# Performance work log

Hardware: AMD Instinct MI355X
Metric: run time of the kernel (lower is better)

## Reference

```python
import jax, jax.numpy as jnp
import numpy as np

EPS = 1e-6

def _rmsnorm(x, w):
    # matches RMSNorm: compute in fp32, cast back, then scale by weight
    dt = x.dtype
    xf = x.astype(jnp.float32)
    var = jnp.mean(xf * xf, axis=-1, keepdims=True)
    xf = xf * jax.lax.rsqrt(var + EPS)
    return xf.astype(dt) * w


def setup_inputs() -> dict:
    key = jax.random.key(0)
    ks = jax.random.split(key, 4)
    B, N, C = 4, 2048, 1024
    H = 16
    D = C // H
    x = jax.random.normal(ks[0], (B, N, C), dtype=jnp.float32)
    W_qkv = jax.random.normal(ks[1], (C, 3 * C), dtype=jnp.float32) * (1.0 / np.sqrt(C))
    b_qkv = jnp.zeros((3 * C,), dtype=jnp.float32)
    W_proj = jax.random.normal(ks[2], (C, C), dtype=jnp.float32) * (1.0 / np.sqrt(C))
    b_proj = jnp.zeros((C,), dtype=jnp.float32)
    qn_w = jnp.ones((D,), dtype=jnp.float32)
    kn_w = jnp.ones((D,), dtype=jnp.float32)
    return {"x": x, "W_qkv": W_qkv, "b_qkv": b_qkv, "W_proj": W_proj,
            "b_proj": b_proj, "qn_w": qn_w, "kn_w": kn_w}


def reference(x, W_qkv, b_qkv, W_proj, b_proj, qn_w, kn_w):
    B, N, C = x.shape
    H = 16
    D = C // H
    qkv = jnp.einsum('bnc,cd->bnd', x, W_qkv) + b_qkv          # [B,N,3C]
    qkv = qkv.reshape(B, N, 3, H, D)
    q = qkv[:, :, 0].transpose(0, 2, 1, 3)                     # [B,H,N,D]
    k = qkv[:, :, 1].transpose(0, 2, 1, 3)
    v = qkv[:, :, 2].transpose(0, 2, 1, 3)
    q = _rmsnorm(q, qn_w)
    k = _rmsnorm(k, kn_w)
    scale = D ** -0.5
    attn = jnp.einsum('bhqd,bhkd->bhqk', q, k) * scale         # [B,H,N,N]
    attn = jax.nn.softmax(attn, axis=-1)
    out = jnp.einsum('bhqk,bhkd->bhqd', attn, v)               # [B,H,N,D]
    out = out.transpose(0, 2, 1, 3).reshape(B, N, C)
    out = jnp.einsum('bnc,cd->bnd', out, W_proj) + b_proj
    return out
```

## Files before the change

### kernel.cpp

```cpp
#include <hip/hip_runtime.h>
#include <stdint.h>

#define B_ 4
#define N_ 2048
#define C_ 1024
#define H_ 16
#define D_ 64
#define M_ (B_*N_)
#define N3_ (3*C_)

typedef __attribute__((ext_vector_type(8))) __bf16 bf16x8;
typedef bf16x8 bf16x8_ma __attribute__((may_alias));
typedef __attribute__((ext_vector_type(4))) float floatx4;
typedef unsigned short u16;
typedef unsigned int u32;

typedef __attribute__((address_space(1))) const void void_g;
typedef __attribute__((address_space(3))) void void_l;

__device__ __forceinline__ void glds16(const void* g, void* l) {
  __builtin_amdgcn_global_load_lds((void_g*)g, (void_l*)l, 16, 0, 0);
}

__device__ __forceinline__ u16 f2bf(float f) {
  union { float f; u32 u; } x; x.f = f;
  u32 r = x.u + 0x7fffu + ((x.u >> 16) & 1u);
  return (u16)(r >> 16);
}

__device__ __forceinline__ float fexp2(float x) {
#if __has_builtin(__builtin_amdgcn_exp2f)
  return __builtin_amdgcn_exp2f(x);
#else
  return exp2f(x);
#endif
}

__global__ __launch_bounds__(256)
void convert_x(const float4* __restrict__ in, uint2* __restrict__ out, int n4) {
  int idx = blockIdx.x * 256 + threadIdx.x;
  if (idx >= n4) return;
  float4 v = in[idx];
  union { u16 a[4]; uint2 u; } p;
  p.a[0] = f2bf(v.x); p.a[1] = f2bf(v.y); p.a[2] = f2bf(v.z); p.a[3] = f2bf(v.w);
  out[idx] = p.u;
}

__global__ __launch_bounds__(256)
void transpose_cvt(const float* __restrict__ in, u16* __restrict__ out,
                   int R, int Ccols) {
  __shared__ u16 tile[64][65];
  int c0 = blockIdx.x * 64, r0 = blockIdx.y * 64;
  int tid = threadIdx.x;
#pragma unroll
  for (int it = 0; it < 16; ++it) {
    int idx = it * 256 + tid;
    int r = idx >> 6, c = idx & 63;
    tile[c][r] = f2bf(in[(size_t)(r0 + r) * Ccols + c0 + c]);
  }
  __syncthreads();
#pragma unroll
  for (int it = 0; it < 16; ++it) {
    int idx = it * 256 + tid;
    int oc = idx >> 6, orr = idx & 63;
    out[(size_t)(c0 + oc) * R + r0 + orr] = tile[oc][orr];
  }
}

__global__ __launch_bounds__(256)
void transpose_v(const u16* __restrict__ qkv, u16* __restrict__ vt) {
  __shared__ u16 tile[64][65];
  int bh = blockIdx.y, b = bh >> 4, h = bh & 15;
  int n0 = blockIdx.x * 64;
  int tid = threadIdx.x;
#pragma unroll
  for (int it = 0; it < 16; ++it) {
    int idx = it * 256 + tid;
    int n = idx >> 6, d = idx & 63;
    tile[d][n] = qkv[(size_t)(b * N_ + n0 + n) * N3_ + 2 * C_ + h * D_ + d];
  }
  __syncthreads();
#pragma unroll
  for (int it = 0; it < 16; ++it) {
    int idx = it * 256 + tid;
    int d = idx >> 6, n = idx & 63;
    int np = (n & 0x23) | ((n & 0x0C) << 1) | ((n & 0x10) >> 2);
    vt[(size_t)(bh * D_ + d) * N_ + n0 + np] = tile[d][n];
  }
}

__global__ __launch_bounds__(512, 2)
void gemm_qkv_256(const u16* __restrict__ A, const u16* __restrict__ Bt,
                  const float* __restrict__ bias, u16* __restrict__ Cout,
                  const float* __restrict__ qn, const float* __restrict__ kn) {
  __shared__ __align__(16) u16 sA[4][16 * 512];
  __shared__ __align__(16) u16 sB[4][16 * 512];
  const int K = C_;
  int tid = threadIdx.x;
  int wave = tid >> 6, lane = tid & 63;
  int lrow = lane & 15, lq = lane >> 4;
  int n0 = blockIdx.x * 256;
  int m0 = blockIdx.y * 256;
  int wm = wave >> 2, wn = wave & 3;

  floatx4 acc[8][4];
#pragma unroll
  for (int i = 0; i < 8; ++i)
#pragma unroll
    for (int j = 0; j < 4; ++j) acc[i][j] = (floatx4){0.f, 0.f, 0.f, 0.f};

  const u16* pa0 = A  + (size_t)(m0 + (2 * wave + 0) * 16 + lrow) * K + lq * 8;
  const u16* pa1 = A  + (size_t)(m0 + (2 * wave + 1) * 16 + lrow) * K + lq * 8;
  const u16* pb0 = Bt + (size_t)(n0 + (2 * wave + 0) * 16 + lrow) * K + lq * 8;
  const u16* pb1 = Bt + (size_t)(n0 + (2 * wave + 1) * 16 + lrow) * K + lq * 8;
  int oa0 = (2 * wave + 0) * 512, oa1 = (2 * wave + 1) * 512;

#define STAGE_HK(hk_)                                   \
  do {                                                  \
    int s_ = (hk_) & 3;                                 \
    int ko_ = (hk_) * 32;                               \
    glds16(pa0 + ko_, &sA[s_][oa0]);                    \
    glds16(pa1 + ko_, &sA[s_][oa1]);                    \
    glds16(pb0 + ko_, &sB[s_][oa0]);                    \
    glds16(pb1 + ko_, &sB[s_][oa1]);                    \
  } while (0)

  STAGE_HK(0); STAGE_HK(1); STAGE_HK(2);

  for (int hk = 0; hk < 32; ++hk) {
    if (hk < 30)       asm volatile("s_waitcnt vmcnt(8)" ::: "memory");
    else if (hk == 30) asm volatile("s_waitcnt vmcnt(4)" ::: "memory");
    else               asm volatile("s_waitcnt vmcnt(0)" ::: "memory");
    __builtin_amdgcn_s_barrier();
    asm volatile("" ::: "memory");

    if (hk + 3 < 32) STAGE_HK(hk + 3);

    int s = hk & 3;
    bf16x8 af[8], bfr[4];
#pragma unroll
    for (int i = 0; i < 8; ++i)
      af[i] = *(const bf16x8_ma*)(&sA[s][(wm * 8 + i) * 512 + lane * 8]);
#pragma unroll
    for (int j = 0; j < 4; ++j)
      bfr[j] = *(const bf16x8_ma*)(&sB[s][(wn * 4 + j) * 512 + lane * 8]);

    __builtin_amdgcn_s_setprio(1);
#pragma unroll
    for (int i = 0; i < 8; ++i)
#pragma unroll
      for (int j = 0; j < 4; ++j)
        acc[i][j] = __builtin_amdgcn_mfma_f32_16x16x32_bf16(af[i], bfr[j], acc[i][j], 0, 0, 0);
    __builtin_amdgcn_s_setprio(0);
  }
#undef STAGE_HK

  int colbase = n0 + wn * 64;
  float bv[4];
#pragma unroll
  for (int j = 0; j < 4; ++j) bv[j] = bias[colbase + j * 16 + lrow];
#pragma unroll
  for (int i = 0; i < 8; ++i)
#pragma unroll
    for (int j = 0; j < 4; ++j)
#pragma unroll
      for (int r = 0; r < 4; ++r) acc[i][j][r] += bv[j];

  int sect = colbase >> 10;
  if (sect < 2) {
    const float* wptr = (sect == 0) ? qn : kn;
    float wv[4];
#pragma unroll
    for (int j = 0; j < 4; ++j) wv[j] = wptr[j * 16 + lrow];
#pragma unroll
    for (int i = 0; i < 8; ++i)
#pragma unroll
      for (int r = 0; r < 4; ++r) {
        float ss = 0.f;
#pragma unroll
        for (int j = 0; j < 4; ++j) { float v = acc[i][j][r]; ss += v * v; }
        ss += __shfl_xor(ss, 1);
        ss += __shfl_xor(ss, 2);
        ss += __shfl_xor(ss, 4);
        ss += __shfl_xor(ss, 8);
        float rstd = rsqrtf(ss * (1.0f / 64.0f) + 1e-6f);
#pragma unroll
        for (int j = 0; j < 4; ++j) acc[i][j][r] *= rstd * wv[j];
      }
  }

#pragma unroll
  for (int i = 0; i < 8; ++i)
#pragma unroll
    for (int j = 0; j < 4; ++j)
#pragma unroll
      for (int r = 0; r < 4; ++r) {
        int row = m0 + wm * 128 + i * 16 + lq * 4 + r;
        int col = colbase + j * 16 + lrow;
        Cout[(size_t)row * N3_ + col] = f2bf(acc[i][j][r]);
      }
}

__global__ __launch_bounds__(256)
void gemm_bt(const u16* __restrict__ A, const u16* __restrict__ Bt,
             const float* __restrict__ bias, void* __restrict__ Cout,
             int Ncols, int lda, int do_rms, int out_fp32,
             const float* __restrict__ qn, const float* __restrict__ kn) {
  __shared__ __align__(16) u16 sA[3][8 * 512];
  __shared__ __align__(16) u16 sB[3][8 * 512];
  const int K = C_;
  int tid = threadIdx.x;
  int wave = tid >> 6, lane = tid & 63;
  int lrow = lane & 15, lq = lane >> 4;
  int n0 = blockIdx.x * 128;
  int m0 = blockIdx.y * 128;
  int wm = wave >> 1, wn = wave & 1;

  floatx4 acc[4][4];
#pragma unroll
  for (int i = 0; i < 4; ++i)
#pragma unroll
    for (int j = 0; j < 4; ++j) acc[i][j] = (floatx4){0.f, 0.f, 0.f, 0.f};

  const u16* ga0 = A  + (size_t)(m0 + (2 * wave + 0) * 16 + lrow) * lda + lq * 8;
  const u16* ga1 = A  + (size_t)(m0 + (2 * wave + 1) * 16 + lrow) * lda + lq * 8;
  const u16* gb0 = Bt + (size_t)(n0 + (2 * wave + 0) * 16 + lrow) * K + lq * 8;
  const u16* gb1 = Bt + (size_t)(n0 + (2 * wave + 1) * 16 + lrow) * K + lq * 8;
  int o0 = (2 * wave + 0) * 512;
  int o1 = (2 * wave + 1) * 512;

  u16* aA = &sA[0][0]; u16* aB = &sA[1][0]; u16* aC = &sA[2][0];
  u16* bA = &sB[0][0]; u16* bB = &sB[1][0]; u16* bC = &sB[2][0];

  glds16(ga0, aA + o0); glds16(ga1, aA + o1);
  glds16(gb0, bA + o0); glds16(gb1, bA + o1);
  glds16(ga0 + 32, aB + o0); glds16(ga1 + 32, aB + o1);
  glds16(gb0 + 32, bB + o0); glds16(gb1 + 32, bB + o1);

  for (int kt = 0; kt < K; kt += 32) {
    if (kt + 32 < K) {
      asm volatile("s_waitcnt vmcnt(4)" ::: "memory");
    } else {
      asm volatile("s_waitcnt vmcnt(0)" ::: "memory");
    }
    __builtin_amdgcn_s_barrier();
    asm volatile("" ::: "memory");

    if (kt + 64 < K) {
      glds16(ga0 + kt + 64, aC + o0);
      glds16(ga1 + kt + 64, aC + o1);
      glds16(gb0 + kt + 64, bC + o0);
      glds16(gb1 + kt + 64, bC + o1);
    }

    bf16x8 af[4], bfr[4];
#pragma unroll
    for (int i = 0; i < 4; ++i)
      af[i] = *(const bf16x8_ma*)(aA + (wm * 4 + i) * 512 + lane * 8);
#pragma unroll
    for (int j = 0; j < 4; ++j)
      bfr[j] = *(const bf16x8_ma*)(bA + (wn * 4 + j) * 512 + lane * 8);
#pragma unroll
    for (int i = 0; i < 4; ++i)
#pragma unroll
      for (int j = 0; j < 4; ++j)
        acc[i][j] = __builtin_amdgcn_mfma_f32_16x16x32_bf16(af[i], bfr[j], acc[i][j], 0, 0, 0);

    u16* t;
    t = aA; aA = aB; aB = aC; aC = t;
    t = bA; bA = bB; bB = bC; bC = t;
  }

  int colbase = n0 + wn * 64;
  float bv[4];
#pragma unroll
  for (int j = 0; j < 4; ++j) bv[j] = bias[colbase + j * 16 + lrow];
#pragma unroll
  for (int i = 0; i < 4; ++i)
#pragma unroll
    for (int j = 0; j < 4; ++j)
#pragma unroll
      for (int r = 0; r < 4; ++r) acc[i][j][r] += bv[j];

  int sect = colbase >> 10;
  if (do_rms && sect < 2) {
    const float* wptr = (sect == 0) ? qn : kn;
    float wv[4];
#pragma unroll
    for (int j = 0; j < 4; ++j) wv[j] = wptr[j * 16 + lrow];
#pragma unroll
    for (int i = 0; i < 4; ++i)
#pragma unroll
      for (int r = 0; r < 4; ++r) {
        float ss = 0.f;
#pragma unroll
        for (int j = 0; j < 4; ++j) { float v = acc[i][j][r]; ss += v * v; }
        ss += __shfl_xor(ss, 1);
        ss += __shfl_xor(ss, 2);
        ss += __shfl_xor(ss, 4);
        ss += __shfl_xor(ss, 8);
        float rstd = rsqrtf(ss * (1.0f / 64.0f) + 1e-6f);
#pragma unroll
        for (int j = 0; j < 4; ++j) acc[i][j][r] *= rstd * wv[j];
      }
  }

#pragma unroll
  for (int i = 0; i < 4; ++i)
#pragma unroll
    for (int j = 0; j < 4; ++j)
#pragma unroll
      for (int r = 0; r < 4; ++r) {
        int row = m0 + wm * 64 + i * 16 + lq * 4 + r;
        int col = colbase + j * 16 + lrow;
        if (out_fp32)
          ((float*)Cout)[(size_t)row * Ncols + col] = acc[i][j][r];
        else
          ((u16*)Cout)[(size_t)row * Ncols + col] = f2bf(acc[i][j][r]);
      }
}

__global__ __launch_bounds__(256)
void flash_attn(u16* __restrict__ qkv, const u16* __restrict__ vt) {
  __shared__ __align__(16) u16 sK[2][8 * 512];
  __shared__ __align__(16) u16 sV[2][8 * 512];
  int tid = threadIdx.x;
  int wave = tid >> 6, lane = tid & 63;
  int lrow = lane & 15, lq = lane >> 4;
  int bh = blockIdx.y, b = bh >> 4, h = bh & 15;
  int q0 = blockIdx.x * 128;
  const float cc = 0.125f * 1.44269504088896340736f;

  bf16x8 qf[2][2];
#pragma unroll
  for (int i = 0; i < 2; ++i)
#pragma unroll
    for (int kq = 0; kq < 2; ++kq) {
      union { bf16x8 v; __bf16 e[8]; } t;
      t.v = *(const bf16x8_ma*)(qkv +
          (size_t)(b * N_ + q0 + wave * 32 + i * 16 + lrow) * N3_ +
          h * D_ + kq * 32 + lq * 8);
#pragma unroll
      for (int e = 0; e < 8; ++e) t.e[e] = (__bf16)((float)t.e[e] * cc);
      qf[i][kq] = t.v;
    }

  union { bf16x8 v; u16 e[8]; } one_;
#pragma unroll
  for (int e = 0; e < 8; ++e) one_.e[e] = 0x3F80;
  bf16x8 onef = one_.v;

  floatx4 aco[2][4];
  floatx4 acl[2];
#pragma unroll
  for (int i = 0; i < 2; ++i) {
#pragma unroll
    for (int nd = 0; nd < 4; ++nd) aco[i][nd] = (floatx4){0.f, 0.f, 0.f, 0.f};
    acl[i] = (floatx4){0.f, 0.f, 0.f, 0.f};
  }

  const u16* gk[2];
  const u16* gv[2];
#pragma unroll
  for (int t = 0; t < 2; ++t) {
    int blk = wave * 2 + t;
    int j = blk >> 1, kq = blk & 1;
    gk[t] = qkv + (size_t)(b * N_ + j * 16 + lrow) * N3_ +
            C_ + h * D_ + kq * 32 + lq * 8;
    gv[t] = vt + (size_t)(bh * D_ + j * 16 + lrow) * N_ + kq * 32 + lq * 8;
  }

  u16* k_cur = &sK[0][0]; u16* k_nxt = &sK[1][0];
  u16* v_cur = &sV[0][0]; u16* v_nxt = &sV[1][0];

#pragma unroll
  for (int t = 0; t < 2; ++t) {
    int blk = wave * 2 + t;
    glds16(gk[t], k_cur + blk * 512);
    glds16(gv[t], v_cur + blk * 512);
  }
  __syncthreads();

  for (int kt = 0; kt < 32; ++kt) {
    if (kt < 31) {
      size_t key0n = (size_t)(kt + 1) * 64;
#pragma unroll
      for (int t = 0; t < 2; ++t) {
        int blk = wave * 2 + t;
        glds16(gk[t] + key0n * N3_, k_nxt + blk * 512);
        glds16(gv[t] + key0n, v_nxt + blk * 512);
      }
    }

    floatx4 accs[2][4];
    __builtin_amdgcn_s_setprio(1);
#pragma unroll
    for (int j = 0; j < 4; ++j) {
      bf16x8 kf0 = *(const bf16x8_ma*)(k_cur + (j * 2 + 0) * 512 + lane * 8);
      bf16x8 kf1 = *(const bf16x8_ma*)(k_cur + (j * 2 + 1) * 512 + lane * 8);
#pragma unroll
      for (int i = 0; i < 2; ++i) {
        floatx4 s = (floatx4){0.f, 0.f, 0.f, 0.f};
        s = __builtin_amdgcn_mfma_f32_16x16x32_bf16(kf0, qf[i][0], s, 0, 0, 0);
        s = __builtin_amdgcn_mfma_f32_16x16x32_bf16(kf1, qf[i][1], s, 0, 0, 0);
        accs[i][j] = s;
      }
    }
    __builtin_amdgcn_s_setprio(0);

    bf16x8 pf[2][2];
#pragma unroll
    for (int i = 0; i < 2; ++i) {
      union { bf16x8 v; __bf16 e[8]; } pk0, pk1;
#pragma unroll
      for (int j = 0; j < 4; ++j)
#pragma unroll
        for (int r = 0; r < 4; ++r) {
          float p = fexp2(accs[i][j][r]);
          if (j < 2) pk0.e[(j & 1) * 4 + r] = (__bf16)p;
          else       pk1.e[(j & 1) * 4 + r] = (__bf16)p;
        }
      pf[i][0] = pk0.v;
      pf[i][1] = pk1.v;
    }

    __builtin_amdgcn_s_setprio(1);
#pragma unroll
    for (int kq = 0; kq < 2; ++kq) {
#pragma unroll
      for (int nd = 0; nd < 4; ++nd) {
        bf16x8 vf = *(const bf16x8_ma*)(v_cur + (nd * 2 + kq) * 512 + lane * 8);
        aco[0][nd] = __builtin_amdgcn_mfma_f32_16x16x32_bf16(vf, pf[0][kq], aco[0][nd], 0, 0, 0);
        aco[1][nd] = __builtin_amdgcn_mfma_f32_16x16x32_bf16(vf, pf[1][kq], aco[1][nd], 0, 0, 0);
      }
      acl[0] = __builtin_amdgcn_mfma_f32_16x16x32_bf16(onef, pf[0][kq], acl[0], 0, 0, 0);
      acl[1] = __builtin_amdgcn_mfma_f32_16x16x32_bf16(onef, pf[1][kq], acl[1], 0, 0, 0);
    }
    __builtin_amdgcn_s_setprio(0);

    __syncthreads();
    u16* t0 = k_cur; k_cur = k_nxt; k_nxt = t0;
    u16* t1 = v_cur; v_cur = v_nxt; v_nxt = t1;
  }

#pragma unroll
  for (int i = 0; i < 2; ++i) {
    float inv = 1.0f / acl[i][0];
    int row = q0 + wave * 32 + i * 16 + lrow;
#pragma unroll
    for (int nd = 0; nd < 4; ++nd) {
      union { u16 a[4]; uint2 u; } st;
#pragma unroll
      for (int r = 0; r < 4; ++r) st.a[r] = f2bf(aco[i][nd][r] * inv);
      *(uint2*)(qkv + (size_t)(b * N_ + row) * N3_ + h * D_ + nd * 16 + lq * 4) = st.u;
    }
  }
}

extern "C" void kernel_launch(void* const* d_in, const int* in_sizes, int n_in,
                              void* d_out, int out_size, void* d_ws, size_t ws_size,
                              hipStream_t stream) {
  (void)in_sizes; (void)n_in; (void)out_size; (void)ws_size;
  const float* x     = (const float*)d_in[0];
  const float* Wqkv  = (const float*)d_in[1];
  const float* bqkv  = (const float*)d_in[2];
  const float* Wproj = (const float*)d_in[3];
  const float* bproj = (const float*)d_in[4];
  const float* qn    = (const float*)d_in[5];
  const float* kn    = (const float*)d_in[6];
  float* out = (float*)d_out;

  char* ws = (char*)d_ws;
  u16* xb      = (u16*)ws;  ws += (size_t)M_ * C_ * 2;
  u16* Wt_qkv  = (u16*)ws;  ws += (size_t)N3_ * C_ * 2;
  u16* Wt_proj = (u16*)ws;  ws += (size_t)C_ * C_ * 2;
  u16* qkv     = (u16*)ws;  ws += (size_t)M_ * N3_ * 2;
  u16* vt      = (u16*)ws;  ws += (size_t)B_ * H_ * D_ * N_ * 2;

  convert_x<<<dim3(M_ * C_ / 4 / 256), 256, 0, stream>>>(
      (const float4*)x, (uint2*)xb, M_ * C_ / 4);
  transpose_cvt<<<dim3(N3_ / 64, C_ / 64), 256, 0, stream>>>(Wqkv, Wt_qkv, C_, N3_);
  transpose_cvt<<<dim3(C_ / 64, C_ / 64), 256, 0, stream>>>(Wproj, Wt_proj, C_, C_);
  gemm_qkv_256<<<dim3(N3_ / 256, M_ / 256), 512, 0, stream>>>(
      xb, Wt_qkv, bqkv, qkv, qn, kn);
  transpose_v<<<dim3(N_ / 64, B_ * H_), 256, 0, stream>>>(qkv, vt);
  flash_attn<<<dim3(N_ / 128, B_ * H_), 256, 0, stream>>>(qkv, vt);
  gemm_bt<<<dim3(C_ / 128, M_ / 128), 256, 0, stream>>>(
      qkv, Wt_proj, bproj, out, C_, N3_, 0, 1, qn, kn);
}
```

Measured before the change: 340.1 us.

## Shrink QKV GEMM tile to 128x256 and add XCD-aware block swizzling

Replaces the 256x256 QKV GEMM, which used a 4-stage pipeline and setprio, with a 128x256 tile on a 3-stage LDS pipeline. This halves the accumulators per wave and doubles the number of workgroups. It also remaps block indices in the projection GEMM and flash attention so that consecutive logical tiles land on the same XCD, aiming for better L2 reuse. The smaller tile lowers arithmetic intensity per block and drops the priority hints, in exchange for more parallelism and lower register pressure.

```diff
diff --git a/kernel.cpp b/kernel.cpp
--- a/kernel.cpp
+++ b/kernel.cpp
@@ -34,6 +34,11 @@
 #else
   return exp2f(x);
 #endif
+}
+
+__device__ __forceinline__ int xcd_swz(int hw, int nwg) {
+  int per = nwg >> 3;
+  return (hw & 7) * per + (hw >> 3);
 }
 
 __global__ __launch_bounds__(256)
@@ -89,78 +94,81 @@
   }
 }
 
-__global__ __launch_bounds__(512, 2)
-void gemm_qkv_256(const u16* __restrict__ A, const u16* __restrict__ Bt,
-                  const float* __restrict__ bias, u16* __restrict__ Cout,
-                  const float* __restrict__ qn, const float* __restrict__ kn) {
-  __shared__ __align__(16) u16 sA[4][16 * 512];
-  __shared__ __align__(16) u16 sB[4][16 * 512];
+__global__ __launch_bounds__(512)
+void gemm_qkv(const u16* __restrict__ A, const u16* __restrict__ Bt,
+              const float* __restrict__ bias, u16* __restrict__ Cout,
+              const float* __restrict__ qn, const float* __restrict__ kn) {
+  __shared__ __align__(16) u16 sA[3][8 * 512];
+  __shared__ __align__(16) u16 sB[3][16 * 512];
   const int K = C_;
   int tid = threadIdx.x;
   int wave = tid >> 6, lane = tid & 63;
   int lrow = lane & 15, lq = lane >> 4;
   int n0 = blockIdx.x * 256;
-  int m0 = blockIdx.y * 256;
+  int m0 = blockIdx.y * 128;
   int wm = wave >> 2, wn = wave & 3;
 
-  floatx4 acc[8][4];
-#pragma unroll
-  for (int i = 0; i < 8; ++i)
+  floatx4 acc[4][4];
+#pragma unroll
+  for (int i = 0; i < 4; ++i)
 #pragma unroll
     for (int j = 0; j < 4; ++j) acc[i][j] = (floatx4){0.f, 0.f, 0.f, 0.f};
 
-  const u16* pa0 = A  + (size_t)(m0 + (2 * wave + 0) * 16 + lrow) * K + lq * 8;
-  const u16* pa1 = A  + (size_t)(m0 + (2 * wave + 1) * 16 + lrow) * K + lq * 8;
-  const u16* pb0 = Bt + (size_t)(n0 + (2 * wave + 0) * 16 + lrow) * K + lq * 8;
-  const u16* pb1 = Bt + (size_t)(n0 + (2 * wave + 1) * 16 + lrow) * K + lq * 8;
-  int oa0 = (2 * wave + 0) * 512, oa1 = (2 * wave + 1) * 512;
-
-#define STAGE_HK(hk_)                                   \
-  do {                                                  \
-    int s_ = (hk_) & 3;                                 \
-    int ko_ = (hk_) * 32;                               \
-    glds16(pa0 + ko_, &sA[s_][oa0]);                    \
-    glds16(pa1 + ko_, &sA[s_][oa1]);                    \
-    glds16(pb0 + ko_, &sB[s_][oa0]);                    \
-    glds16(pb1 + ko_, &sB[s_][oa1]);                    \
+  const u16* ga  = A  + (size_t)(m0 + wave * 16 + lrow) * K + lq * 8;
+  const u16* gb0 = Bt + (size_t)(n0 + (2 * wave + 0) * 16 + lrow) * K + lq * 8;
+  const u16* gb1 = Bt + (size_t)(n0 + (2 * wave + 1) * 16 + lrow) * K + lq * 8;
+  int oa  = wave * 512;
+  int ob0 = (2 * wave + 0) * 512;
+  int ob1 = (2 * wave + 1) * 512;
+
+#define STAGE(kt_, s_)                      \
+  do {                                      \
+    glds16(ga  + (kt_), &sA[s_][oa]);       \
+    glds16(gb0 + (kt_), &sB[s_][ob0]);      \
+    glds16(gb1 + (kt_), &sB[s_][ob1]);      \
   } while (0)
 
-  STAGE_HK(0); STAGE_HK(1); STAGE_HK(2);
-
-  for (int hk = 0; hk < 32; ++hk) {
-    if (hk < 30)       asm volatile("s_waitcnt vmcnt(8)" ::: "memory");
-    else if (hk == 30) asm volatile("s_waitcnt vmcnt(4)" ::: "memory");
-    else               asm volatile("s_waitcnt vmcnt(0)" ::: "memory");
+  STAGE(0, 0);
+  STAGE(32, 1);
+
+  int slot = 0;
+  for (int kt = 0; kt < K; kt += 32) {
+    if (kt + 32 < K) {
+      asm volatile("s_waitcnt vmcnt(3)" ::: "memory");
+    } else {
+      asm volatile("s_waitcnt vmcnt(0)" ::: "memory");
+    }
     __builtin_amdgcn_s_barrier();
     asm volatile("" ::: "memory");
 
-    if (hk + 3 < 32) STAGE_HK(hk + 3);
-
-    int s = hk & 3;
-    bf16x8 af[8], bfr[4];
-#pragma unroll
-    for (int i = 0; i < 8; ++i)
-      af[i] = *(const bf16x8_ma*)(&sA[s][(wm * 8 + i) * 512 + lane * 8]);
+    if (kt + 64 < K) {
+      int s2 = slot + 2; if (s2 >= 3) s2 -= 3;
+      STAGE(kt + 64, s2);
+    }
+
+    bf16x8 af[4], bfr[4];
+#pragma unroll
+    for (int i = 0; i < 4; ++i)
+      af[i] = *(const bf16x8_ma*)(&sA[slot][(wm * 4 + i) * 512 + lane * 8]);
 #pragma unroll
     for (int j = 0; j < 4; ++j)
-      bfr[j] = *(const bf16x8_ma*)(&sB[s][(wn * 4 + j) * 512 + lane * 8]);
-
-    __builtin_amdgcn_s_setprio(1);
-#pragma unroll
-    for (int i = 0; i < 8; ++i)
+      bfr[j] = *(const bf16x8_ma*)(&sB[slot][(wn * 4 + j) * 512 + lane * 8]);
+#pragma unroll
+    for (int i = 0; i < 4; ++i)
 #pragma unroll
       for (int j = 0; j < 4; ++j)
         acc[i][j] = __builtin_amdgcn_mfma_f32_16x16x32_bf16(af[i], bfr[j], acc[i][j], 0, 0, 0);
-    __builtin_amdgcn_s_setprio(0);
-  }
-#undef STAGE_HK
+
+    ++slot; if (slot >= 3) slot = 0;
+  }
+#undef STAGE
 
   int colbase = n0 + wn * 64;
   float bv[4];
 #pragma unroll
   for (int j = 0; j < 4; ++j) bv[j] = bias[colbase + j * 16 + lrow];
 #pragma unroll
-  for (int i = 0; i < 8; ++i)
+  for (int i = 0; i < 4; ++i)
 #pragma unroll
     for (int j = 0; j < 4; ++j)
 #pragma unroll
@@ -173,7 +181,7 @@
 #pragma unroll
     for (int j = 0; j < 4; ++j) wv[j] = wptr[j * 16 + lrow];
 #pragma unroll
-    for (int i = 0; i < 8; ++i)
+    for (int i = 0; i < 4; ++i)
 #pragma unroll
       for (int r = 0; r < 4; ++r) {
         float ss = 0.f;
@@ -190,12 +198,12 @@
   }
 
 #pragma unroll
-  for (int i = 0; i < 8; ++i)
+  for (int i = 0; i < 4; ++i)
 #pragma unroll
     for (int j = 0; j < 4; ++j)
 #pragma unroll
       for (int r = 0; r < 4; ++r) {
-        int row = m0 + wm * 128 + i * 16 + lq * 4 + r;
+        int row = m0 + wm * 64 + i * 16 + lq * 4 + r;
         int col = colbase + j * 16 + lrow;
         Cout[(size_t)row * N3_ + col] = f2bf(acc[i][j][r]);
       }
@@ -212,8 +220,13 @@
   int tid = threadIdx.x;
   int wave = tid >> 6, lane = tid & 63;
   int lrow = lane & 15, lq = lane >> 4;
-  int n0 = blockIdx.x * 128;
-  int m0 = blockIdx.y * 128;
+
+  int nwg = gridDim.x * gridDim.y;
+  int hw = blockIdx.y * gridDim.x + blockIdx.x;
+  int lg = xcd_swz(hw, nwg);
+  int bx = lg % gridDim.x, by = lg / gridDim.x;
+  int n0 = bx * 128;
+  int m0 = by * 128;
   int wm = wave >> 1, wn = wave & 1;
 
   floatx4 acc[4][4];
@@ -327,8 +340,12 @@
   int tid = threadIdx.x;
   int wave = tid >> 6, lane = tid & 63;
   int lrow = lane & 15, lq = lane >> 4;
-  int bh = blockIdx.y, b = bh >> 4, h = bh & 15;
-  int q0 = blockIdx.x * 128;
+
+  int hw = blockIdx.y * gridDim.x + blockIdx.x;
+  int lg = xcd_swz(hw, 1024);
+  int qblk = lg & 15, bh = lg >> 4;
+  int b = bh >> 4, h = bh & 15;
+  int q0 = qblk * 128;
   const float cc = 0.125f * 1.44269504088896340736f;
 
   bf16x8 qf[2][2];
@@ -481,7 +498,7 @@
       (const float4*)x, (uint2*)xb, M_ * C_ / 4);
   transpose_cvt<<<dim3(N3_ / 64, C_ / 64), 256, 0, stream>>>(Wqkv, Wt_qkv, C_, N3_);
   transpose_cvt<<<dim3(C_ / 64, C_ / 64), 256, 0, stream>>>(Wproj, Wt_proj, C_, C_);
-  gemm_qkv_256<<<dim3(N3_ / 256, M_ / 256), 512, 0, stream>>>(
+  gemm_qkv<<<dim3(N3_ / 256, M_ / 128), 512, 0, stream>>>(
       xb, Wt_qkv, bqkv, qkv, qn, kn);
   transpose_v<<<dim3(N_ / 64, B_ * H_), 256, 0, stream>>>(qkv, vt);
   flash_attn<<<dim3(N_ / 128, B_ * H_), 256, 0, stream>>>(qkv, vt);
```

Result: faster. 317.9 us (-6.5%).
